# Optimization experiments

Hardware: AMD Instinct MI355X
Metric: run time of the kernel (lower is better)

Reference implementation:

```python
import math
import jax, jax.numpy as jnp
import numpy as np

NB, NF, NTS = 16, 512, 2048
FREQ_START, FREQ_END = 0.1, 10.0
C = 1.0 / (8.0 * math.pi ** 2)


def setup_inputs() -> dict:
    key = jax.random.key(0)
    k1, k2 = jax.random.split(key)
    ys = jax.random.normal(k1, (NB, NTS), dtype=jnp.float32)
    # irregular but monotonically increasing time stamps in [0, NTS)
    ts = jnp.sort(jax.random.uniform(k2, (NB, NTS), dtype=jnp.float32,
                                     minval=0.0, maxval=float(NTS)), axis=1)
    freq = jnp.linspace(FREQ_START, FREQ_END, NF, dtype=jnp.float32)
    return {"ys": ys, "ts": ts, "freq": freq}


def reference(ys, ts, freq):
    nts = ts.shape[1]
    # center of the window: midpoint of the two central samples -> [B,1,1]
    tau = (0.5 * (ts[:, nts // 2] + ts[:, nts // 2 + 1]))[:, None, None]
    omega = freq * (2.0 * math.pi)            # [F]
    omega_ = omega[None, :, None]             # [1,F,1]
    ts_ = ts[:, None, :]                      # [B,1,T]
    ys_ = ys[:, None, :]                      # [B,1,T]

    dz = omega_ * (ts_ - tau)                 # [B,F,T]
    weights = jnp.exp(-C * dz * dz)           # shared Gaussian window [B,F,T]
    sum_w = jnp.sum(weights, axis=-1)         # [B,F]

    def w_mean(x):
        return jnp.sum(weights * x, axis=-1) / sum_w

    theta = omega_ * ts_
    sin_basis = jnp.sin(theta)
    cos_basis = jnp.cos(theta)

    sin_one = w_mean(sin_basis)
    cos_one = w_mean(cos_basis)
    sin_cos = w_mean(sin_basis * cos_basis)
    sin_sin = w_mean(sin_basis * sin_basis)
    cos_cos = w_mean(cos_basis * cos_basis)

    numerator = 2.0 * (sin_cos - sin_one * cos_one)
    denominator = cos_cos - cos_one ** 2 - (sin_sin - sin_one ** 2)
    time_shift = jnp.arctan2(numerator, denominator) / (2.0 * omega)  # [B,F]

    phase_arg = omega_ * (ts_ - time_shift[:, :, None])
    sin_shift = jnp.sin(phase_arg)
    cos_shift = jnp.cos(phase_arg)
    sin_tau_center = jnp.sin(omega * (time_shift - tau[:, :, 0]))  # [B,F]
    cos_tau_center = jnp.cos(omega * (time_shift - tau[:, :, 0]))

    ys_cos_shift = w_mean(ys_ * cos_shift)
    ys_sin_shift = w_mean(ys_ * sin_shift)
    ys_one = w_mean(ys_)
    cos_shift_one = w_mean(cos_shift)
    sin_shift_one = w_mean(sin_shift)

    A = 2.0 * (ys_cos_shift - ys_one * cos_shift_one)
    B = 2.0 * (ys_sin_shift - ys_one * sin_shift_one)

    a0 = ys_one
    a1 = cos_tau_center * A - sin_tau_center * B
    a2 = sin_tau_center * A + cos_tau_center * B
    wwp = a1 ** 2 + a2 ** 2
    phase = jnp.arctan2(a2, a1)
    return (wwp, phase, a0, a1, a2)
```

## Files before the change

kernel.cpp:

```cpp
#include <hip/hip_runtime.h>
#include <math.h>

namespace {
constexpr int kNB  = 16;
constexpr int kNF  = 512;
constexpr int kNTS = 2048;
constexpr int kTPB = 256;
constexpr int kEPT = kNTS / kTPB;
constexpr int kVPT = kEPT / 4;
constexpr float kC     = 0.012665147955292222f;
constexpr float kTwoPi = 6.28318530717958647692f;

constexpr float kTwoOverPi = 0.636619772367581343f;
constexpr float kP1 = 1.5703125f;
constexpr float kP2 = 4.84466552734375e-4f;
constexpr float kP3 = -6.407499313354492e-7f;
constexpr float kP4 = 9.895302355289459e-10f;
}

__device__ __forceinline__ void fast_sincosf(float x, float& s_out, float& c_out) {
  float kf = rintf(x * kTwoOverPi);
  int   q  = (int)kf;
  float r  = fmaf(-kf, kP1, x);
  r = fmaf(-kf, kP2, r);
  r = fmaf(-kf, kP3, r);
  r = fmaf(-kf, kP4, r);

  float z = r * r;
  float sp = fmaf(fmaf(-1.9515295891e-4f, z, 8.3321608736e-3f), z, -1.6666654611e-1f);
  float s  = fmaf(sp * z, r, r);
  float cp = fmaf(fmaf(2.443315711809948e-5f, z, -1.388731625493765e-3f), z,
                  4.166664568298827e-2f);
  float c  = fmaf(cp, z * z, fmaf(-0.5f, z, 1.0f));

  bool sw = (q & 1) != 0;
  float ss = sw ? c : s;
  float cc = sw ? s : c;
  unsigned sgn_s = (unsigned)(q & 2) << 30;
  unsigned sgn_c = (unsigned)((q + 1) & 2) << 30;
  s_out = __uint_as_float(__float_as_uint(ss) ^ sgn_s);
  c_out = __uint_as_float(__float_as_uint(cc) ^ sgn_c);
}

__launch_bounds__(kTPB, 4)
__global__ void wavelet_ls_kernel(const float* __restrict__ ys,
                                  const float* __restrict__ ts,
                                  const float* __restrict__ freq,
                                  float* __restrict__ out) {
  const int f    = blockIdx.x;
  const int b    = blockIdx.y;
  const int tid  = threadIdx.x;
  const int wave = tid >> 6;

  const float* __restrict__ tsb = ts + b * kNTS;
  const float* __restrict__ ysb = ys + b * kNTS;
  const float4* __restrict__ ts4 = (const float4*)tsb;
  const float4* __restrict__ ys4 = (const float4*)ysb;

  const float tau   = 0.5f * (tsb[kNTS / 2] + tsb[kNTS / 2 + 1]);
  const float omega = freq[f] * kTwoPi;

  float tv[kEPT], wv[kEPT], wyv[kEPT];

  float acc[6];
#pragma unroll
  for (int i = 0; i < 6; ++i) acc[i] = 0.0f;

#pragma unroll
  for (int v = 0; v < kVPT; ++v) {
    const int vidx = v * kTPB + tid;
    const float4 t4 = ts4[vidx];
    const float4 y4 = ys4[vidx];
    const float te[4] = {t4.x, t4.y, t4.z, t4.w};
    const float ye[4] = {y4.x, y4.y, y4.z, y4.w};
#pragma unroll
    for (int j = 0; j < 4; ++j) {
      const int k = v * 4 + j;
      const float t = te[j];
      const float y = ye[j];
      tv[k] = t;
      const float dz = omega * (t - tau);
      const float e  = (-kC * dz) * dz;
      const float w  = __expf(e);
      wv[k]  = w;
      wyv[k] = w * y;
      float sn, cs;
      fast_sincosf(omega * t, sn, cs);
      const float c2 = fmaf(-2.0f * sn, sn, 1.0f);
      acc[0] += w;
      acc[1] = fmaf(w, sn, acc[1]);
      acc[2] = fmaf(w, cs, acc[2]);
      acc[3] = fmaf(w, sn * cs, acc[3]);
      acc[4] = fmaf(w, c2, acc[4]);
      acc[5] = fmaf(w, y, acc[5]);
    }
  }

  __shared__ float lds1[4][6];
#pragma unroll
  for (int i = 0; i < 6; ++i) {
    float v = acc[i];
#pragma unroll
    for (int off = 1; off < 64; off <<= 1) v += __shfl_xor(v, off, 64);
    if ((tid & 63) == 0) lds1[wave][i] = v;
  }
  __syncthreads();

  float tot[6];
#pragma unroll
  for (int i = 0; i < 6; ++i)
    tot[i] = (lds1[0][i] + lds1[1][i]) + (lds1[2][i] + lds1[3][i]);

  const float sum_w   = tot[0];
  const float inv_w   = 1.0f / sum_w;
  const float sin_one = tot[1] * inv_w;
  const float cos_one = tot[2] * inv_w;
  const float sin_cos = tot[3] * inv_w;
  const float cc_ss   = tot[4] * inv_w;
  const float ys_one  = tot[5] * inv_w;

  const float num = 2.0f * (sin_cos - sin_one * cos_one);
  const float den = cc_ss - cos_one * cos_one + sin_one * sin_one;
  const float time_shift = atan2f(num, den) / (2.0f * omega);

  float a20 = 0.0f, a21 = 0.0f, a22 = 0.0f, a23 = 0.0f;
#pragma unroll
  for (int k = 0; k < kEPT; ++k) {
    float sn, cs;
    fast_sincosf(omega * (tv[k] - time_shift), sn, cs);
    const float w  = wv[k];
    const float wy = wyv[k];
    a20 = fmaf(w,  cs, a20);
    a21 = fmaf(w,  sn, a21);
    a22 = fmaf(wy, cs, a22);
    a23 = fmaf(wy, sn, a23);
  }

  __shared__ float lds2[4][4];
  {
    float av[4] = {a20, a21, a22, a23};
#pragma unroll
    for (int i = 0; i < 4; ++i) {
      float v = av[i];
#pragma unroll
      for (int off = 1; off < 64; off <<= 1) v += __shfl_xor(v, off, 64);
      if ((tid & 63) == 0) lds2[wave][i] = v;
    }
  }
  __syncthreads();

  if (tid == 0) {
    float t2[4];
#pragma unroll
    for (int i = 0; i < 4; ++i)
      t2[i] = (lds2[0][i] + lds2[1][i]) + (lds2[2][i] + lds2[3][i]);

    const float cos_shift_one = t2[0] * inv_w;
    const float sin_shift_one = t2[1] * inv_w;
    const float ys_cos_shift  = t2[2] * inv_w;
    const float ys_sin_shift  = t2[3] * inv_w;

    float stc, ctc;
    sincosf(omega * (time_shift - tau), &stc, &ctc);

    const float A  = 2.0f * (ys_cos_shift - ys_one * cos_shift_one);
    const float B  = 2.0f * (ys_sin_shift - ys_one * sin_shift_one);
    const float a0 = ys_one;
    const float a1 = ctc * A - stc * B;
    const float a2 = stc * A + ctc * B;
    const float wwp   = a1 * a1 + a2 * a2;
    const float phase = atan2f(a2, a1);

    const int o = b * kNF + f;
    out[0 * kNB * kNF + o] = wwp;
    out[1 * kNB * kNF + o] = phase;
    out[2 * kNB * kNF + o] = a0;
    out[3 * kNB * kNF + o] = a1;
    out[4 * kNB * kNF + o] = a2;
  }
}

extern "C" void kernel_launch(void* const* d_in, const int* in_sizes, int n_in,
                              void* d_out, int out_size, void* d_ws, size_t ws_size,
                              hipStream_t stream) {
  const float* ys   = (const float*)d_in[0];
  const float* ts   = (const float*)d_in[1];
  const float* freq = (const float*)d_in[2];
  float* out = (float*)d_out;

  dim3 grid(kNF, kNB);
  wavelet_ls_kernel<<<grid, kTPB, 0, stream>>>(ys, ts, freq, out);
}
```

Before: 39.23 us.

## Process two frequency bins per block with 128-thread groups and use exp2

Each 256-thread block now handles two (batch, frequency) bins, giving 128 threads per bin and 16 samples per thread instead of 8. Blocks are halved, and each wave's reduction covers more work per sync, lowering per-block and per-reduction overhead. The Gaussian weight is now computed with the native exp2 builtin and a pre-scaled constant rather than __expf. Holding twice the samples in per-thread register arrays raises register pressure, which may cut occupancy under the launch bounds.

Measured after the change: 45.32 us. 1.16x slower.

```diff
diff --git a/kernel.cpp b/kernel.cpp
--- a/kernel.cpp
+++ b/kernel.cpp
@@ -6,9 +6,12 @@
 constexpr int kNF  = 512;
 constexpr int kNTS = 2048;
 constexpr int kTPB = 256;
-constexpr int kEPT = kNTS / kTPB;
+constexpr int kBinsPerBlock = 2;
+constexpr int kTPG = kTPB / kBinsPerBlock;
+constexpr int kEPT = kNTS / kTPG;
 constexpr int kVPT = kEPT / 4;
 constexpr float kC     = 0.012665147955292222f;
+constexpr float kCL2   = 0.0182719460f;
 constexpr float kTwoPi = 6.28318530717958647692f;
 
 constexpr float kTwoOverPi = 0.636619772367581343f;
@@ -47,10 +50,13 @@
                                   const float* __restrict__ ts,
                                   const float* __restrict__ freq,
                                   float* __restrict__ out) {
-  const int f    = blockIdx.x;
-  const int b    = blockIdx.y;
-  const int tid  = threadIdx.x;
-  const int wave = tid >> 6;
+  const int tid   = threadIdx.x;
+  const int group = tid >> 7;
+  const int gtid  = tid & (kTPG - 1);
+  const int gwave = (tid >> 6) & 1;
+  const int bin   = blockIdx.x * kBinsPerBlock + group;
+  const int b     = bin >> 9;
+  const int f     = bin & (kNF - 1);
 
   const float* __restrict__ tsb = ts + b * kNTS;
   const float* __restrict__ ysb = ys + b * kNTS;
@@ -68,7 +74,7 @@
 
 #pragma unroll
   for (int v = 0; v < kVPT; ++v) {
-    const int vidx = v * kTPB + tid;
+    const int vidx = v * kTPG + gtid;
     const float4 t4 = ts4[vidx];
     const float4 y4 = ys4[vidx];
     const float te[4] = {t4.x, t4.y, t4.z, t4.w};
@@ -80,8 +86,8 @@
       const float y = ye[j];
       tv[k] = t;
       const float dz = omega * (t - tau);
-      const float e  = (-kC * dz) * dz;
-      const float w  = __expf(e);
+      const float e2 = (-kCL2 * dz) * dz;
+      const float w  = __builtin_amdgcn_exp2f(e2);
       wv[k]  = w;
       wyv[k] = w * y;
       float sn, cs;
@@ -96,20 +102,20 @@
     }
   }
 
-  __shared__ float lds1[4][6];
+  __shared__ float lds1[kBinsPerBlock][2][6];
 #pragma unroll
   for (int i = 0; i < 6; ++i) {
     float v = acc[i];
 #pragma unroll
     for (int off = 1; off < 64; off <<= 1) v += __shfl_xor(v, off, 64);
-    if ((tid & 63) == 0) lds1[wave][i] = v;
+    if ((tid & 63) == 0) lds1[group][gwave][i] = v;
   }
   __syncthreads();
 
   float tot[6];
 #pragma unroll
   for (int i = 0; i < 6; ++i)
-    tot[i] = (lds1[0][i] + lds1[1][i]) + (lds1[2][i] + lds1[3][i]);
+    tot[i] = lds1[group][0][i] + lds1[group][1][i];
 
   const float sum_w   = tot[0];
   const float inv_w   = 1.0f / sum_w;
@@ -136,7 +142,7 @@
     a23 = fmaf(wy, sn, a23);
   }
 
-  __shared__ float lds2[4][4];
+  __shared__ float lds2[kBinsPerBlock][2][4];
   {
     float av[4] = {a20, a21, a22, a23};
 #pragma unroll
@@ -144,16 +150,16 @@
       float v = av[i];
 #pragma unroll
       for (int off = 1; off < 64; off <<= 1) v += __shfl_xor(v, off, 64);
-      if ((tid & 63) == 0) lds2[wave][i] = v;
+      if ((tid & 63) == 0) lds2[group][gwave][i] = v;
     }
   }
   __syncthreads();
 
-  if (tid == 0) {
+  if (gtid == 0) {
     float t2[4];
 #pragma unroll
     for (int i = 0; i < 4; ++i)
-      t2[i] = (lds2[0][i] + lds2[1][i]) + (lds2[2][i] + lds2[3][i]);
+      t2[i] = lds2[group][0][i] + lds2[group][1][i];
 
     const float cos_shift_one = t2[0] * inv_w;
     const float sin_shift_one = t2[1] * inv_w;
@@ -188,6 +194,6 @@
   const float* freq = (const float*)d_in[2];
   float* out = (float*)d_out;
 
-  dim3 grid(kNF, kNB);
+  dim3 grid(kNB * kNF / kBinsPerBlock);
   wavelet_ls_kernel<<<grid, kTPB, 0, stream>>>(ys, ts, freq, out);
 }
```
